# Performance work log

Hardware: AMD Instinct MI355X
Metric: run time of the kernel (lower is better)

The kernel has to match this reference:

```python
import jax, jax.numpy as jnp
import numpy as np

TOP_K = 4  # top_k_neighbors from __init__


def setup_inputs() -> dict:
    key = jax.random.key(0)
    k1, k2, k3, k4 = jax.random.split(key, 4)
    R, B, D, N = 256, 64, 512, 16
    h = jax.random.normal(k1, (R, B, D), dtype=jnp.float32)
    nbrs = jax.random.randint(k2, (R, N), 0, R, dtype=jnp.int32)
    W_msg = jax.random.normal(k3, (D, D), dtype=jnp.float32) * 0.02
    b_msg = jnp.zeros((D,), dtype=jnp.float32)
    W_merge = jax.random.normal(k4, (D, 2 * D), dtype=jnp.float32) * 0.02
    b_merge = jnp.zeros((D,), dtype=jnp.float32)
    return {
        "h_by_region": h,
        "neighbor_indices": nbrs,
        "W_msg": W_msg,
        "b_msg": b_msg,
        "W_merge": W_merge,
        "b_merge": b_merge,
    }


def reference(h_by_region, neighbor_indices, W_msg, b_msg, W_merge, b_merge):
    # h_by_region: [R, B, D]; neighbor_indices: [R, N] int32
    R, B, D = h_by_region.shape
    h = h_by_region
    # sim(r, j) = mean over (B, D) of h[r] * h[j]. Compute the full Gram once
    # ([R, R], tiny) instead of materializing [R, N, B, D] just for sims.
    G = jnp.einsum('rbd,sbd->rs', h, h) / (B * D)
    sims = jnp.take_along_axis(G, neighbor_indices, axis=1)           # [R, N]
    _, top = jax.lax.top_k(sims, TOP_K)                               # [R, K]
    sel = jnp.take_along_axis(neighbor_indices, top, axis=1)          # [R, K]
    # Gather selected neighbor states, project to messages, average over K.
    h_sel = h[sel]                                                    # [R, K, B, D]
    msgs = jnp.einsum('rkbd,ed->rkbe', h_sel, W_msg) + b_msg          # [R, K, B, D]
    m = msgs.mean(axis=1)                                             # [R, B, D]
    cat = jnp.concatenate([h, m], axis=-1)                            # [R, B, 2D]
    out = jnp.einsum('rbf,ef->rbe', cat, W_merge) + b_merge           # [R, B, D]
    avg_fanin = jnp.float32(TOP_K)  # every region keeps exactly top_k neighbors
    return out, avg_fanin
```

## Files before the change

### kernel.cpp

```cpp
#include <hip/hip_runtime.h>
#include <hip/hip_bf16.h>

#define R_ 256
#define B_ 64
#define D_ 512
#define N_ 16
#define K_ 4
#define RBD (B_ * D_)
#define OUT_ELEMS (R_ * B_ * D_)
#define M_TOT (R_ * B_)
#define GSLICES 64
#define GPAIRS 10
#define GBLK (GSLICES * GPAIRS)

typedef __attribute__((address_space(1))) unsigned int g_u32;
typedef __attribute__((address_space(3))) unsigned int l_u32;
using f32x4 = __attribute__((ext_vector_type(4))) float;
using f16x8 = __attribute__((ext_vector_type(8))) _Float16;
using f16x4 = __attribute__((ext_vector_type(4))) _Float16;

__constant__ int kBx[GPAIRS] = {0, 0, 0, 0, 1, 1, 1, 2, 2, 3};
__constant__ int kBy[GPAIRS] = {0, 1, 2, 3, 1, 2, 3, 2, 3, 3};

__global__ __launch_bounds__(256, 4) void gramx_kernel(
    const float* __restrict__ h, const float* __restrict__ Wm,
    const float* __restrict__ Wmsg, _Float16* __restrict__ A16,
    float* __restrict__ Cp, float* __restrict__ W2p) {
  __shared__ char smem[32768];
  const int t = threadIdx.x;
  const int bid = blockIdx.x;

  if (bid >= GBLK) {
    const int gid = bid - GBLK;
    const int db = (gid & 15) * 32;
    const int eb = ((gid >> 4) & 15) * 32;
    const int kc = gid >> 8;
    float(*As)[33] = (float(*)[33])smem;
    float(*Bs)[33] = (float(*)[33])(smem + 32 * 33 * 4);
    const int tx = t % 16, ty = t / 16;
    const int lr = t / 8;
    const int lc = (t % 8) * 4;
    float a00 = 0.f, a01 = 0.f, a10 = 0.f, a11 = 0.f;
    for (int c0 = kc * 128; c0 < kc * 128 + 128; c0 += 32) {
      float4 av = *(const float4*)&Wm[(size_t)(eb + lr) * 1024 + 512 + c0 + lc];
      float4 bv = *(const float4*)&Wmsg[(size_t)(c0 + lr) * 512 + db + lc];
      As[lr][lc + 0] = av.x; As[lr][lc + 1] = av.y;
      As[lr][lc + 2] = av.z; As[lr][lc + 3] = av.w;
      Bs[lr][lc + 0] = bv.x; Bs[lr][lc + 1] = bv.y;
      Bs[lr][lc + 2] = bv.z; Bs[lr][lc + 3] = bv.w;
      __syncthreads();
#pragma unroll
      for (int kk = 0; kk < 32; kk++) {
        float x0 = As[2 * ty + 0][kk], x1 = As[2 * ty + 1][kk];
        float y0 = Bs[kk][2 * tx + 0], y1 = Bs[kk][2 * tx + 1];
        a00 += x0 * y0; a01 += x0 * y1;
        a10 += x1 * y0; a11 += x1 * y1;
      }
      __syncthreads();
    }
    float* base = W2p + (size_t)kc * 512 * 512;
    base[(size_t)(eb + 2 * ty + 0) * 512 + db + 2 * tx + 0] = a00;
    base[(size_t)(eb + 2 * ty + 0) * 512 + db + 2 * tx + 1] = a01;
    base[(size_t)(eb + 2 * ty + 1) * 512 + db + 2 * tx + 0] = a10;
    base[(size_t)(eb + 2 * ty + 1) * 512 + db + 2 * tx + 1] = a11;
    return;
  }

  const int work = (bid & 7) * (GBLK / 8) + (bid >> 3);
  const int s = work / GPAIRS;
  const int pr = work % GPAIRS;
  const int bx = kBx[pr];
  const int by = kBy[pr];
  const int I = bx * 64;
  const int J = by * 64;
  const bool duty = (bx == by);
  const int lane = t & 63;
  const int w = t >> 6;
  char* sHiI = smem;
  char* sHiJ = smem + 8192;
  char* sLoJ = smem + 16384;
  char* sLoI = smem + 24576;
  const int wm = w >> 1, wn = w & 1;
  const int rlane = lane & 15;
  const int kq = lane >> 4;

  f32x4 c1[2][2] = {};
  f32x4 c2[2][2] = {};
  f32x4 c3[2][2] = {};

  const float* hI = h + (size_t)I * RBD + (size_t)s * 512;
  const float* hJ = h + (size_t)J * RBD + (size_t)s * 512;
  const int frow = t >> 4;
  const int fc4 = t & 15;

  float4 rI[4], rJ[4];
#pragma unroll
  for (int u = 0; u < 4; ++u) {
    const int row = u * 16 + frow;
    rI[u] = *(const float4*)&hI[(size_t)row * RBD + fc4 * 4];
    rJ[u] = *(const float4*)&hJ[(size_t)row * RBD + fc4 * 4];
  }

  for (int kt = 0; kt < 8; ++kt) {
    if (kt) __syncthreads();
#pragma unroll
    for (int u = 0; u < 4; ++u) {
      const int row = u * 16 + frow;
      const int boff =
          row * 128 + (((fc4 >> 1) ^ (row & 7)) << 4) + (fc4 & 1) * 8;
      float4 vI = rI[u];
      f16x4 hiI = {(_Float16)vI.x, (_Float16)vI.y, (_Float16)vI.z,
                   (_Float16)vI.w};
      f16x4 loI = {(_Float16)(vI.x - (float)hiI[0]),
                   (_Float16)(vI.y - (float)hiI[1]),
                   (_Float16)(vI.z - (float)hiI[2]),
                   (_Float16)(vI.w - (float)hiI[3])};
      *(f16x4*)(sHiI + boff) = hiI;
      *(f16x4*)(sLoI + boff) = loI;
      float4 vJ = rJ[u];
      f16x4 hiJ = {(_Float16)vJ.x, (_Float16)vJ.y, (_Float16)vJ.z,
                   (_Float16)vJ.w};
      f16x4 loJ = {(_Float16)(vJ.x - (float)hiJ[0]),
                   (_Float16)(vJ.y - (float)hiJ[1]),
                   (_Float16)(vJ.z - (float)hiJ[2]),
                   (_Float16)(vJ.w - (float)hiJ[3])};
      *(f16x4*)(sHiJ + boff) = hiJ;
      *(f16x4*)(sLoJ + boff) = loJ;
      if (duty)
        *(f16x4*)&A16[(size_t)(J + row) * RBD + (size_t)s * 512 + kt * 64 +
                      fc4 * 4] = hiJ;
    }
    __syncthreads();
    if (kt < 7) {
#pragma unroll
      for (int u = 0; u < 4; ++u) {
        const int row = u * 16 + frow;
        rI[u] =
            *(const float4*)&hI[(size_t)row * RBD + (kt + 1) * 64 + fc4 * 4];
        rJ[u] =
            *(const float4*)&hJ[(size_t)row * RBD + (kt + 1) * 64 + fc4 * 4];
      }
    }
#pragma unroll
    for (int ks = 0; ks < 2; ++ks) {
      f16x8 ai[2], li[2], bj[2], lj[2];
#pragma unroll
      for (int i = 0; i < 2; ++i) {
        const int row = wm * 32 + i * 16 + rlane;
        const int slot = (ks * 4 + kq) ^ (row & 7);
        ai[i] = *(const f16x8*)(sHiI + row * 128 + slot * 16);
        li[i] = *(const f16x8*)(sLoI + row * 128 + slot * 16);
      }
#pragma unroll
      for (int j = 0; j < 2; ++j) {
        const int row = wn * 32 + j * 16 + rlane;
        const int slot = (ks * 4 + kq) ^ (row & 7);
        bj[j] = *(const f16x8*)(sHiJ + row * 128 + slot * 16);
        lj[j] = *(const f16x8*)(sLoJ + row * 128 + slot * 16);
      }
#pragma unroll
      for (int i = 0; i < 2; ++i)
#pragma unroll
        for (int j = 0; j < 2; ++j) {
          c1[i][j] = __builtin_amdgcn_mfma_f32_16x16x32_f16(ai[i], bj[j],
                                                            c1[i][j], 0, 0, 0);
          c2[i][j] = __builtin_amdgcn_mfma_f32_16x16x32_f16(ai[i], lj[j],
                                                            c2[i][j], 0, 0, 0);
          c3[i][j] = __builtin_amdgcn_mfma_f32_16x16x32_f16(li[i], bj[j],
                                                            c3[i][j], 0, 0, 0);
        }
    }
  }

  f32x4 cs[2][2];
#pragma unroll
  for (int i = 0; i < 2; ++i)
#pragma unroll
    for (int j = 0; j < 2; ++j)
      cs[i][j] = c1[i][j] + c2[i][j] + c3[i][j];

#pragma unroll
  for (int i = 0; i < 2; ++i) {
#pragma unroll
    for (int reg = 0; reg < 4; ++reg) {
      const int gr = I + wm * 32 + i * 16 + kq * 4 + reg;
      const size_t base = ((size_t)s * 256 + gr) * 256 + J + wn * 32 + rlane;
#pragma unroll
      for (int j = 0; j < 2; ++j) Cp[base + j * 16] = cs[i][j][reg];
    }
  }
  if (!duty) {
#pragma unroll
    for (int i = 0; i < 2; ++i)
#pragma unroll
      for (int j = 0; j < 2; ++j) {
        const int gc = J + wn * 32 + j * 16 + rlane;
        const int gr0 = I + wm * 32 + i * 16 + kq * 4;
        *(f32x4*)&Cp[((size_t)s * 256 + gc) * 256 + gr0] = cs[i][j];
      }
  }
}

__global__ __launch_bounds__(256) void fin_kernel(
    const float* __restrict__ Cp, const int* __restrict__ nbrs,
    const float* __restrict__ W2p, const float* __restrict__ Wm,
    const float* __restrict__ b_msg, const float* __restrict__ b_merge,
    const _Float16* __restrict__ A16, _Float16* __restrict__ Am16,
    int* __restrict__ sel, float* __restrict__ fanin,
    _Float16* __restrict__ W16, float* __restrict__ bias_eff) {
  const int bx = blockIdx.x;
  const int t = threadIdx.x;
  if (bx < 256) {
    const int r = bx;
    __shared__ float sims_all[256];
    __shared__ int nb_s[N_];
    __shared__ int sel_sm[K_];
    const float* base = Cp + (size_t)r * 256 + t;
    float acc = 0.f;
#pragma unroll 8
    for (int s = 0; s < GSLICES; ++s) acc += base[(size_t)s * 65536];
    sims_all[t] = acc;
    if (t < N_) nb_s[t] = nbrs[r * N_ + t];
    __syncthreads();
    if (t == 0) {
      float sims_s[N_];
#pragma unroll
      for (int n = 0; n < N_; ++n) sims_s[n] = sims_all[nb_s[n]];
      unsigned used = 0;
#pragma unroll
      for (int k = 0; k < K_; k++) {
        float best = -3.0e38f;
        int bi = 0;
        for (int nn = 0; nn < N_; nn++) {
          if (used & (1u << nn)) continue;
          float vv = sims_s[nn];
          if (vv > best) { best = vv; bi = nn; }
        }
        used |= 1u << bi;
        const int sj = nb_s[bi];
        sel[r * K_ + k] = sj;
        sel_sm[k] = sj;
      }
      if (r == 0) *fanin = 4.0f;
    }
    __syncthreads();
    const _Float16* g0 = A16 + (size_t)sel_sm[0] * RBD;
    const _Float16* g1 = A16 + (size_t)sel_sm[1] * RBD;
    const _Float16* g2 = A16 + (size_t)sel_sm[2] * RBD;
    const _Float16* g3 = A16 + (size_t)sel_sm[3] * RBD;
    _Float16* dst = Am16 + (size_t)r * RBD;
#pragma unroll 4
    for (int i = t; i < RBD / 8; i += 256) {
      const size_t off = (size_t)i * 8;
      f16x8 q0 = *(const f16x8*)&g0[off];
      f16x8 q1 = *(const f16x8*)&g1[off];
      f16x8 q2 = *(const f16x8*)&g2[off];
      f16x8 q3 = *(const f16x8*)&g3[off];
      f16x8 m = ((q0 + q1) + (q2 + q3)) * (_Float16)0.25f;
      *(f16x8*)&dst[off] = m;
    }
  } else if (bx < 1280) {
    const int i = (bx - 256) * 256 + t;
    const int e = i >> 9;
    const int d = i & 511;
    float acc = 0.f;
#pragma unroll
    for (int kc = 0; kc < 4; ++kc)
      acc += W2p[(size_t)kc * 512 * 512 + (size_t)e * 512 + d];
    W16[(size_t)e * 1024 + 512 + d] = (_Float16)acc;
  } else if (bx < 1536) {
    const int i = (bx - 1280) * 256 + t;
    const int e = i >> 7;
    const int c4 = (i & 127) * 4;
    float4 v = *(const float4*)&Wm[(size_t)e * 1024 + c4];
    f16x4 o = {(_Float16)v.x, (_Float16)v.y, (_Float16)v.z, (_Float16)v.w};
    *(f16x4*)&W16[(size_t)e * 1024 + c4] = o;
  } else {
    const int e = (bx - 1536) * 256 + t;
    const float4* bp = (const float4*)b_msg;
    const float4* wp = (const float4*)&Wm[(size_t)e * 1024 + 512];
    float acc = 0.f;
    for (int c = 0; c < 128; c++) {
      float4 b4 = bp[c], w4 = wp[c];
      acc += b4.x * w4.x + b4.y * w4.y + b4.z * w4.z + b4.w * w4.w;
    }
    bias_eff[e] = acc + b_merge[e];
  }
}

__global__ __launch_bounds__(256, 4) void mfma_gemm_kernel(
    const _Float16* __restrict__ A16, const _Float16* __restrict__ Am16,
    const _Float16* __restrict__ W16, const float* __restrict__ bias,
    float* __restrict__ out) {
  const int t = threadIdx.x;
  const int lane = t & 63;
  const int w = t >> 6;
  const int bid = blockIdx.x;
  const int work = (bid & 7) * 128 + (bid >> 3);
  const int eb = (work & 3) * 128;
  const int my = work >> 2;
  const int m0 = my * 64;
  __shared__ char smemA[64 * 128];
  __shared__ char smemW[128 * 128];
  const int wm = w >> 1, wn = w & 1;
  const int rlane = lane & 15;
  const int kq = lane >> 4;

  f32x4 acc[2][4] = {};

  const char* Ab = (const char*)A16;
  const char* Amb = (const char*)Am16;
  const char* Wb = (const char*)W16;

  for (int kt = 0; kt < 16; ++kt) {
#pragma unroll
    for (int u = 0; u < 2; ++u) {
      const int f = u * 256 + t;
      const int row = f >> 3;
      const int slot = (f & 7) ^ (row & 7);
      const char* ga =
          (kt < 8)
              ? Ab + ((size_t)(m0 + row) * 1024 + kt * 128 + slot * 16)
              : Amb + ((size_t)(m0 + row) * 1024 + (kt - 8) * 128 + slot * 16);
      char* la = smemA + u * 4096 + w * 1024;
      __builtin_amdgcn_global_load_lds((const g_u32*)ga, (l_u32*)la, 16, 0, 0);
    }
#pragma unroll
    for (int q = 0; q < 4; ++q) {
      const int f = q * 256 + t;
      const int row = f >> 3;
      const int slot = (f & 7) ^ (row & 7);
      const char* gw = Wb + ((size_t)(eb + row) * 2048 + kt * 128 + slot * 16);
      char* lw = smemW + q * 4096 + w * 1024;
      __builtin_amdgcn_global_load_lds((const g_u32*)gw, (l_u32*)lw, 16, 0, 0);
    }
    __syncthreads();
#pragma unroll
    for (int ks = 0; ks < 2; ++ks) {
      f16x8 a[2], b[4];
#pragma unroll
      for (int i = 0; i < 2; ++i) {
        const int row = wm * 32 + i * 16 + rlane;
        const int slot = (ks * 4 + kq) ^ (row & 7);
        a[i] = *(const f16x8*)(smemA + row * 128 + slot * 16);
      }
#pragma unroll
      for (int j = 0; j < 4; ++j) {
        const int row = wn * 64 + j * 16 + rlane;
        const int slot = (ks * 4 + kq) ^ (row & 7);
        b[j] = *(const f16x8*)(smemW + row * 128 + slot * 16);
      }
#pragma unroll
      for (int i = 0; i < 2; ++i)
#pragma unroll
        for (int j = 0; j < 4; ++j)
          acc[i][j] = __builtin_amdgcn_mfma_f32_16x16x32_f16(a[i], b[j],
                                                             acc[i][j], 0, 0, 0);
    }
    __syncthreads();
  }

  float bj[4];
#pragma unroll
  for (int j = 0; j < 4; ++j) bj[j] = bias[eb + wn * 64 + j * 16 + rlane];
#pragma unroll
  for (int i = 0; i < 2; ++i) {
#pragma unroll
    for (int reg = 0; reg < 4; ++reg) {
      const size_t m = (size_t)m0 + wm * 32 + i * 16 + kq * 4 + reg;
      float* po = out + m * 512 + eb + wn * 64 + rlane;
#pragma unroll
      for (int j = 0; j < 4; ++j) po[j * 16] = acc[i][j][reg] + bj[j];
    }
  }
}

__global__ __launch_bounds__(256) void bias_kernel(
    const float* __restrict__ Wm, const float* __restrict__ b_msg,
    const float* __restrict__ b_merge, float* __restrict__ bias_eff) {
  const int e = blockIdx.x * 256 + threadIdx.x;
  const float4* bp = (const float4*)b_msg;
  const float4* wp = (const float4*)&Wm[(size_t)e * 1024 + 512];
  float acc = 0.f;
  for (int c = 0; c < 128; c++) {
    float4 b4 = bp[c], w4 = wp[c];
    acc += b4.x * w4.x + b4.y * w4.y + b4.z * w4.z + b4.w * w4.w;
  }
  bias_eff[e] = acc + b_merge[e];
}

__global__ __launch_bounds__(256) void sims_topk_kernel(
    const float* __restrict__ h, const int* __restrict__ nbrs,
    int* __restrict__ sel, float* __restrict__ fanin) {
  const int r = blockIdx.x;
  const int t = threadIdx.x;
  const int lane = t & 63;
  const int wave = t >> 6;
  __shared__ float sims_s[N_];
  __shared__ int nb_s[N_];
  if (t < N_) nb_s[t] = nbrs[r * N_ + t];
  __syncthreads();
  const int n0 = wave * 4;
  const float4* hr  = (const float4*)(h + (size_t)r * RBD);
  const float4* hn0 = (const float4*)(h + (size_t)nb_s[n0 + 0] * RBD);
  const float4* hn1 = (const float4*)(h + (size_t)nb_s[n0 + 1] * RBD);
  const float4* hn2 = (const float4*)(h + (size_t)nb_s[n0 + 2] * RBD);
  const float4* hn3 = (const float4*)(h + (size_t)nb_s[n0 + 3] * RBD);
  float a0 = 0.f, a1 = 0.f, a2 = 0.f, a3 = 0.f;
  for (int i = lane; i < RBD / 4; i += 64) {
    float4 x = hr[i];
    float4 y0 = hn0[i], y1 = hn1[i], y2 = hn2[i], y3 = hn3[i];
    a0 += x.x * y0.x + x.y * y0.y + x.z * y0.z + x.w * y0.w;
    a1 += x.x * y1.x + x.y * y1.y + x.z * y1.z + x.w * y1.w;
    a2 += x.x * y2.x + x.y * y2.y + x.z * y2.z + x.w * y2.w;
    a3 += x.x * y3.x + x.y * y3.y + x.z * y3.z + x.w * y3.w;
  }
  float v[4] = {a0, a1, a2, a3};
#pragma unroll
  for (int n = 0; n < 4; n++) {
    float x = v[n];
#pragma unroll
    for (int off = 32; off > 0; off >>= 1) x += __shfl_down(x, off);
    if (lane == 0) sims_s[n0 + n] = x;
  }
  __syncthreads();
  if (t == 0) {
    unsigned used = 0;
#pragma unroll
    for (int k = 0; k < K_; k++) {
      float best = -3.0e38f;
      int bi = 0;
      for (int n = 0; n < N_; n++) {
        if (used & (1u << n)) continue;
        float vv = sims_s[n];
        if (vv > best) { best = vv; bi = n; }
      }
      used |= 1u << bi;
      sel[r * K_ + k] = nb_s[bi];
    }
    if (r == 0) *fanin = 4.0f;
  }
}

__global__ __launch_bounds__(256) void w2eff_f32_kernel(
    const float* __restrict__ Wm, const float* __restrict__ Wmsg,
    float* __restrict__ W2) {
  __shared__ float As[32][33];
  __shared__ float Bs[32][33];
  const int t = threadIdx.x;
  const int eb = blockIdx.y * 32;
  const int db = blockIdx.x * 32;
  const int tx = t % 16, ty = t / 16;
  const int lr = t / 8;
  const int lc = (t % 8) * 4;
  float a00 = 0.f, a01 = 0.f, a10 = 0.f, a11 = 0.f;
  for (int c0 = 0; c0 < 512; c0 += 32) {
    float4 av = *(const float4*)&Wm[(size_t)(eb + lr) * 1024 + 512 + c0 + lc];
    float4 bv = *(const float4*)&Wmsg[(size_t)(c0 + lr) * 512 + db + lc];
    As[lr][lc + 0] = av.x; As[lr][lc + 1] = av.y;
    As[lr][lc + 2] = av.z; As[lr][lc + 3] = av.w;
    Bs[lr][lc + 0] = bv.x; Bs[lr][lc + 1] = bv.y;
    Bs[lr][lc + 2] = bv.z; Bs[lr][lc + 3] = bv.w;
    __syncthreads();
#pragma unroll
    for (int kk = 0; kk < 32; kk++) {
      float x0 = As[2 * ty + 0][kk], x1 = As[2 * ty + 1][kk];
      float y0 = Bs[kk][2 * tx + 0], y1 = Bs[kk][2 * tx + 1];
      a00 += x0 * y0; a01 += x0 * y1;
      a10 += x1 * y0; a11 += x1 * y1;
    }
    __syncthreads();
  }
  W2[(size_t)(eb + 2 * ty + 0) * 512 + db + 2 * tx + 0] = a00;
  W2[(size_t)(eb + 2 * ty + 0) * 512 + db + 2 * tx + 1] = a01;
  W2[(size_t)(eb + 2 * ty + 1) * 512 + db + 2 * tx + 0] = a10;
  W2[(size_t)(eb + 2 * ty + 1) * 512 + db + 2 * tx + 1] = a11;
}

__global__ __launch_bounds__(256) void fused_gemm_f32_kernel(
    const float* __restrict__ h, const int* __restrict__ sel,
    const float* __restrict__ Wm, const float* __restrict__ W2,
    const float* __restrict__ bias_eff, float* __restrict__ out) {
  const int r = blockIdx.y;
  const int eb = blockIdx.x * 256;
  const int t = threadIdx.x;
  __shared__ float As[64][33];
  __shared__ float Ws[256][33];
  __shared__ int sel_s[K_];
  if (t < K_) sel_s[t] = sel[r * K_ + t];
  __syncthreads();
  const size_t hr = (size_t)r * RBD;
  const size_t s0 = (size_t)sel_s[0] * RBD;
  const size_t s1 = (size_t)sel_s[1] * RBD;
  const size_t s2 = (size_t)sel_s[2] * RBD;
  const size_t s3 = (size_t)sel_s[3] * RBD;
  const int tb = t % 8;
  const int te = t / 8;
  const int ab = t / 4;
  const int ac = (t % 4) * 8;
  float acc[8][8] = {};
  for (int d0 = 0; d0 < 1024; d0 += 32) {
    if (d0 < 512) {
      const float* src = h + hr + (size_t)ab * 512 + d0 + ac;
      float4 v0 = *(const float4*)(src);
      float4 v1 = *(const float4*)(src + 4);
      As[ab][ac + 0] = v0.x; As[ab][ac + 1] = v0.y;
      As[ab][ac + 2] = v0.z; As[ab][ac + 3] = v0.w;
      As[ab][ac + 4] = v1.x; As[ab][ac + 5] = v1.y;
      As[ab][ac + 6] = v1.z; As[ab][ac + 7] = v1.w;
    } else {
      const size_t off = (size_t)ab * 512 + (d0 - 512) + ac;
      const float* p0 = h + s0 + off;
      const float* p1 = h + s1 + off;
      const float* p2 = h + s2 + off;
      const float* p3 = h + s3 + off;
      float4 q0 = *(const float4*)p0, q0b = *(const float4*)(p0 + 4);
      float4 q1 = *(const float4*)p1, q1b = *(const float4*)(p1 + 4);
      float4 q2 = *(const float4*)p2, q2b = *(const float4*)(p2 + 4);
      float4 q3 = *(const float4*)p3, q3b = *(const float4*)(p3 + 4);
      As[ab][ac + 0] = 0.25f * (q0.x + q1.x + q2.x + q3.x);
      As[ab][ac + 1] = 0.25f * (q0.y + q1.y + q2.y + q3.y);
      As[ab][ac + 2] = 0.25f * (q0.z + q1.z + q2.z + q3.z);
      As[ab][ac + 3] = 0.25f * (q0.w + q1.w + q2.w + q3.w);
      As[ab][ac + 4] = 0.25f * (q0b.x + q1b.x + q2b.x + q3b.x);
      As[ab][ac + 5] = 0.25f * (q0b.y + q1b.y + q2b.y + q3b.y);
      As[ab][ac + 6] = 0.25f * (q0b.z + q1b.z + q2b.z + q3b.z);
      As[ab][ac + 7] = 0.25f * (q0b.w + q1b.w + q2b.w + q3b.w);
    }
    {
      const float* src = (d0 < 512)
          ? (Wm + (size_t)(eb + t) * 1024 + d0)
          : (W2 + (size_t)(eb + t) * 512 + (d0 - 512));
#pragma unroll
      for (int j = 0; j < 8; j++) {
        float4 v = *(const float4*)(src + 4 * j);
        Ws[t][4 * j + 0] = v.x; Ws[t][4 * j + 1] = v.y;
        Ws[t][4 * j + 2] = v.z; Ws[t][4 * j + 3] = v.w;
      }
    }
    __syncthreads();
#pragma unroll
    for (int kk = 0; kk < 32; kk++) {
      float a[8], wv[8];
#pragma unroll
      for (int i = 0; i < 8; i++) a[i] = As[tb + 8 * i][kk];
#pragma unroll
      for (int j = 0; j < 8; j++) wv[j] = Ws[te + 32 * j][kk];
#pragma unroll
      for (int i = 0; i < 8; i++)
#pragma unroll
        for (int j = 0; j < 8; j++) acc[i][j] += a[i] * wv[j];
    }
    __syncthreads();
  }
  float be[8];
#pragma unroll
  for (int j = 0; j < 8; j++) be[j] = bias_eff[eb + te + 32 * j];
#pragma unroll
  for (int i = 0; i < 8; i++) {
    const int b = tb + 8 * i;
#pragma unroll
    for (int j = 0; j < 8; j++) {
      const int e = eb + te + 32 * j;
      out[hr + (size_t)b * 512 + e] = acc[i][j] + be[j];
    }
  }
}

extern "C" void kernel_launch(void* const* d_in, const int* in_sizes, int n_in,
                              void* d_out, int out_size, void* d_ws,
                              size_t ws_size, hipStream_t stream) {
  const float* h       = (const float*)d_in[0];
  const int*   nbrs    = (const int*)d_in[1];
  const float* W_msg   = (const float*)d_in[2];
  const float* b_msg   = (const float*)d_in[3];
  const float* W_merge = (const float*)d_in[4];
  const float* b_merge = (const float*)d_in[5];
  float* out = (float*)d_out;
  char* ws = (char*)d_ws;

  const size_t SZ_PART = (size_t)GSLICES * 256 * 256 * 4;
  const size_t SZ_A = (size_t)M_TOT * 512 * 2;
  const size_t SZ_W = (size_t)512 * 1024 * 2;
  const size_t SZ_W2P = (size_t)4 * 512 * 512 * 4;
  size_t off = 0;
  int*      sel      = (int*)(ws + off);      off += 4096;
  float*    bias_eff = (float*)(ws + off);    off += 4096;
  float*    Cp       = (float*)(ws + off);    off += SZ_PART;
  _Float16* A16      = (_Float16*)(ws + off); off += SZ_A;
  _Float16* Am16     = (_Float16*)(ws + off); off += SZ_A;
  _Float16* W16      = (_Float16*)(ws + off); off += SZ_W;
  float*    W2p      = (float*)(ws + off);    off += SZ_W2P;
  const size_t NEED = off;

  if (ws_size >= NEED) {
    gramx_kernel<<<GBLK + 1024, 256, 0, stream>>>(h, W_merge, W_msg, A16, Cp,
                                                  W2p);
    fin_kernel<<<1538, 256, 0, stream>>>(Cp, nbrs, W2p, W_merge, b_msg,
                                         b_merge, A16, Am16, sel,
                                         out + OUT_ELEMS, W16, bias_eff);
    mfma_gemm_kernel<<<1024, 256, 0, stream>>>(A16, Am16, W16, bias_eff, out);
  } else {
    int*   fsel     = (int*)ws;
    float* W2       = (float*)(ws + 4096);
    float* fbias    = (float*)(ws + 4096 + 512 * 512 * 4);
    sims_topk_kernel<<<R_, 256, 0, stream>>>(h, nbrs, fsel, out + OUT_ELEMS);
    bias_kernel<<<2, 256, 0, stream>>>(W_merge, b_msg, b_merge, fbias);
    w2eff_f32_kernel<<<dim3(16, 16), 256, 0, stream>>>(W_merge, W_msg, W2);
    fused_gemm_f32_kernel<<<dim3(2, R_), 256, 0, stream>>>(h, fsel, W_merge,
                                                           W2, fbias, out);
  }
}
```

Baseline: 80.21 us.

## Halve Gram K-slices and move weight cast and bias work into first kernel

The Gram split-K partial count is halved (32 slices of 1024 columns instead of 64 of 512), so each gram block runs 16 k-steps and the partial buffer that fin_kernel must reduce shrinks by half. The W_merge left-half fp16 cast and the effective-bias computation move from fin_kernel into extra blocks of gramx_kernel, where they no longer depend on the Gram result. This shortens the serial fin_kernel stage and overlaps independent weight prep with the Gram work, at the cost of fewer gram blocks and less parallelism there.

```diff
diff --git a/kernel.cpp b/kernel.cpp
--- a/kernel.cpp
+++ b/kernel.cpp
@@ -9,7 +9,7 @@
 #define RBD (B_ * D_)
 #define OUT_ELEMS (R_ * B_ * D_)
 #define M_TOT (R_ * B_)
-#define GSLICES 64
+#define GSLICES 32
 #define GPAIRS 10
 #define GBLK (GSLICES * GPAIRS)
 
@@ -24,13 +24,36 @@
 
 __global__ __launch_bounds__(256, 4) void gramx_kernel(
     const float* __restrict__ h, const float* __restrict__ Wm,
-    const float* __restrict__ Wmsg, _Float16* __restrict__ A16,
-    float* __restrict__ Cp, float* __restrict__ W2p) {
+    const float* __restrict__ Wmsg, const float* __restrict__ b_msg,
+    const float* __restrict__ b_merge, _Float16* __restrict__ A16,
+    float* __restrict__ Cp, float* __restrict__ W2p,
+    _Float16* __restrict__ W16, float* __restrict__ bias_eff) {
   __shared__ char smem[32768];
   const int t = threadIdx.x;
   const int bid = blockIdx.x;
 
   if (bid >= GBLK) {
+    if (bid >= 1600) {
+      const int e = (bid - 1600) * 256 + t;
+      const float4* bp = (const float4*)b_msg;
+      const float4* wp = (const float4*)&Wm[(size_t)e * 1024 + 512];
+      float acc = 0.f;
+      for (int c = 0; c < 128; c++) {
+        float4 b4 = bp[c], w4 = wp[c];
+        acc += b4.x * w4.x + b4.y * w4.y + b4.z * w4.z + b4.w * w4.w;
+      }
+      bias_eff[e] = acc + b_merge[e];
+      return;
+    }
+    if (bid >= 1344) {
+      const int i = (bid - 1344) * 256 + t;
+      const int e = i >> 7;
+      const int c4 = (i & 127) * 4;
+      float4 v = *(const float4*)&Wm[(size_t)e * 1024 + c4];
+      f16x4 o = {(_Float16)v.x, (_Float16)v.y, (_Float16)v.z, (_Float16)v.w};
+      *(f16x4*)&W16[(size_t)e * 1024 + c4] = o;
+      return;
+    }
     const int gid = bid - GBLK;
     const int db = (gid & 15) * 32;
     const int eb = ((gid >> 4) & 15) * 32;
@@ -88,8 +111,8 @@
   f32x4 c2[2][2] = {};
   f32x4 c3[2][2] = {};
 
-  const float* hI = h + (size_t)I * RBD + (size_t)s * 512;
-  const float* hJ = h + (size_t)J * RBD + (size_t)s * 512;
+  const float* hI = h + (size_t)I * RBD + (size_t)s * 1024;
+  const float* hJ = h + (size_t)J * RBD + (size_t)s * 1024;
   const int frow = t >> 4;
   const int fc4 = t & 15;
 
@@ -101,7 +124,7 @@
     rJ[u] = *(const float4*)&hJ[(size_t)row * RBD + fc4 * 4];
   }
 
-  for (int kt = 0; kt < 8; ++kt) {
+  for (int kt = 0; kt < 16; ++kt) {
     if (kt) __syncthreads();
 #pragma unroll
     for (int u = 0; u < 4; ++u) {
@@ -127,11 +150,11 @@
       *(f16x4*)(sHiJ + boff) = hiJ;
       *(f16x4*)(sLoJ + boff) = loJ;
       if (duty)
-        *(f16x4*)&A16[(size_t)(J + row) * RBD + (size_t)s * 512 + kt * 64 +
+        *(f16x4*)&A16[(size_t)(J + row) * RBD + (size_t)s * 1024 + kt * 64 +
                       fc4 * 4] = hiJ;
     }
     __syncthreads();
-    if (kt < 7) {
+    if (kt < 15) {
 #pragma unroll
       for (int u = 0; u < 4; ++u) {
         const int row = u * 16 + frow;
@@ -203,11 +226,9 @@
 
 __global__ __launch_bounds__(256) void fin_kernel(
     const float* __restrict__ Cp, const int* __restrict__ nbrs,
-    const float* __restrict__ W2p, const float* __restrict__ Wm,
-    const float* __restrict__ b_msg, const float* __restrict__ b_merge,
-    const _Float16* __restrict__ A16, _Float16* __restrict__ Am16,
-    int* __restrict__ sel, float* __restrict__ fanin,
-    _Float16* __restrict__ W16, float* __restrict__ bias_eff) {
+    const float* __restrict__ W2p, const _Float16* __restrict__ A16,
+    _Float16* __restrict__ Am16, int* __restrict__ sel,
+    float* __restrict__ fanin, _Float16* __restrict__ W16) {
   const int bx = blockIdx.x;
   const int t = threadIdx.x;
   if (bx < 256) {
@@ -259,7 +280,7 @@
       f16x8 m = ((q0 + q1) + (q2 + q3)) * (_Float16)0.25f;
       *(f16x8*)&dst[off] = m;
     }
-  } else if (bx < 1280) {
+  } else {
     const int i = (bx - 256) * 256 + t;
     const int e = i >> 9;
     const int d = i & 511;
@@ -268,23 +289,6 @@
     for (int kc = 0; kc < 4; ++kc)
       acc += W2p[(size_t)kc * 512 * 512 + (size_t)e * 512 + d];
     W16[(size_t)e * 1024 + 512 + d] = (_Float16)acc;
-  } else if (bx < 1536) {
-    const int i = (bx - 1280) * 256 + t;
-    const int e = i >> 7;
-    const int c4 = (i & 127) * 4;
-    float4 v = *(const float4*)&Wm[(size_t)e * 1024 + c4];
-    f16x4 o = {(_Float16)v.x, (_Float16)v.y, (_Float16)v.z, (_Float16)v.w};
-    *(f16x4*)&W16[(size_t)e * 1024 + c4] = o;
-  } else {
-    const int e = (bx - 1536) * 256 + t;
-    const float4* bp = (const float4*)b_msg;
-    const float4* wp = (const float4*)&Wm[(size_t)e * 1024 + 512];
-    float acc = 0.f;
-    for (int c = 0; c < 128; c++) {
-      float4 b4 = bp[c], w4 = wp[c];
-      acc += b4.x * w4.x + b4.y * w4.y + b4.z * w4.z + b4.w * w4.w;
-    }
-    bias_eff[e] = acc + b_merge[e];
   }
 }
 
@@ -594,11 +598,10 @@
   const size_t NEED = off;
 
   if (ws_size >= NEED) {
-    gramx_kernel<<<GBLK + 1024, 256, 0, stream>>>(h, W_merge, W_msg, A16, Cp,
-                                                  W2p);
-    fin_kernel<<<1538, 256, 0, stream>>>(Cp, nbrs, W2p, W_merge, b_msg,
-                                         b_merge, A16, Am16, sel,
-                                         out + OUT_ELEMS, W16, bias_eff);
+    gramx_kernel<<<1602, 256, 0, stream>>>(h, W_merge, W_msg, b_msg, b_merge,
+                                           A16, Cp, W2p, W16, bias_eff);
+    fin_kernel<<<1280, 256, 0, stream>>>(Cp, nbrs, W2p, A16, Am16, sel,
+                                         out + OUT_ELEMS, W16);
     mfma_gemm_kernel<<<1024, 256, 0, stream>>>(A16, Am16, W16, bias_eff, out);
   } else {
     int*   fsel     = (int*)ws;
```

Result: faster. 78.18 us (-2.5%).
